# Optimization experiments

Hardware: AMD Instinct MI355X
Metric: run time of the kernel (lower is better)

Reference implementation:

```python
import jax, jax.numpy as jnp
import numpy as np

N_NODES = 50000
IN_CH = 512
OUT_CH = 512
N_EDGES = 800000


def setup_inputs() -> dict:
    key = jax.random.key(0)
    ks = jax.random.split(key, 6)
    x = jax.random.normal(ks[0], (N_NODES, IN_CH), dtype=jnp.float32)
    edge_index = jax.random.randint(ks[1], (2, N_EDGES), 0, N_NODES, dtype=jnp.int64)
    edge_index_2 = jax.random.randint(ks[2], (2, N_EDGES), 0, N_NODES, dtype=jnp.int64)
    W1 = jax.random.normal(ks[3], (IN_CH, OUT_CH), dtype=jnp.float32) * (1.0 / np.sqrt(IN_CH))
    b1 = jnp.zeros((OUT_CH,), dtype=jnp.float32)
    W2 = jax.random.normal(ks[4], (IN_CH, OUT_CH), dtype=jnp.float32) * (1.0 / np.sqrt(IN_CH))
    b2 = jnp.zeros((OUT_CH,), dtype=jnp.float32)
    return {"x": x, "edge_index": edge_index, "edge_index_2": edge_index_2,
            "W1": W1, "b1": b1, "W2": W2, "b2": b2}


def _sgconv(x, edge_index, W, b, K=2):
    # PyG SGConv: K rounds of D^-1/2 (A+I) D^-1/2 propagation, then Linear.
    N = x.shape[0]
    loops = jnp.arange(N, dtype=edge_index.dtype)
    row = jnp.concatenate([edge_index[0], loops])  # source nodes
    col = jnp.concatenate([edge_index[1], loops])  # destination nodes
    deg = jax.ops.segment_sum(jnp.ones_like(col, dtype=x.dtype), col, num_segments=N)
    deg_inv_sqrt = jnp.where(deg > 0, jnp.where(deg > 0, deg, 1.0) ** -0.5, 0.0)
    norm = deg_inv_sqrt[row] * deg_inv_sqrt[col]  # [E+N]
    h = x
    for _ in range(K):
        h = jax.ops.segment_sum(h[row] * norm[:, None], col, num_segments=N)
    return h @ W + b


def reference(x, edge_index, edge_index_2, W1, b1, W2, b2):
    x1 = _sgconv(x, edge_index, W1, b1)
    x2 = _sgconv(x, edge_index_2, W2, b2)
    logits = jax.nn.softmax(x1, axis=1)
    logits_2 = jax.nn.softmax(x2, axis=1)
    predictions = jnp.argmax(logits, axis=1)
    return (logits, logits_2, predictions)
```

## Files before the change

kernel.cpp:

```cpp
#include <hip/hip_runtime.h>
#include <hip/hip_bf16.h>
#include <cstdint>
#include <cstddef>

#define N_NODES 50000
#define N_EDGES 800000
#define CH 512
#define SCAN_NB 49

typedef __attribute__((ext_vector_type(8))) short bf16x8;
typedef __attribute__((ext_vector_type(4))) float f32x4;

__device__ inline unsigned short f2b(float f) {
    __hip_bfloat16 h = __float2bfloat16(f);
    return *(unsigned short*)&h;
}
__device__ inline float blo(unsigned int u) {
    union { unsigned int i; float f; } v; v.i = u << 16; return v.f;
}
__device__ inline float bhi(unsigned int u) {
    union { unsigned int i; float f; } v; v.i = u & 0xffff0000u; return v.f;
}
__device__ inline unsigned int pack2(unsigned short a, unsigned short b) {
    return (unsigned)a | ((unsigned)b << 16);
}


__global__ __launch_bounds__(256) void count_both(const int* __restrict__ e1, const int* __restrict__ e2,
                                                  int* __restrict__ cnt1, int* __restrict__ cnt2) {
    int t = blockIdx.x * 256 + threadIdx.x;
    if (t < N_EDGES) {
        atomicAdd(&cnt1[e1[N_EDGES + t]], 1);
    } else if (t < 2 * N_EDGES) {
        int e = t - N_EDGES;
        atomicAdd(&cnt2[e2[N_EDGES + e]], 1);
    }
}

__global__ __launch_bounds__(256) void scan_s1(const int* __restrict__ c1, const int* __restrict__ c2,
                                               int* __restrict__ o1, int* __restrict__ o2,
                                               int* __restrict__ bsum) {
    const int* cnt = blockIdx.y ? c2 : c1;
    int* offs = blockIdx.y ? o2 : o1;
    int* bs = bsum + blockIdx.y * 64;
    int b = blockIdx.x, tid = threadIdx.x;
    int lane = tid & 63, wid = tid >> 6;
    int i0 = b * 1024 + tid * 4;
    int v[4];
    #pragma unroll
    for (int j = 0; j < 4; ++j) { int i = i0 + j; v[j] = (i < N_NODES) ? cnt[i] : 0; }
    int tsum = v[0] + v[1] + v[2] + v[3];
    int incl = tsum;
    #pragma unroll
    for (int d = 1; d < 64; d <<= 1) {
        int t = __shfl_up(incl, d, 64);
        if (lane >= d) incl += t;
    }
    __shared__ int wsum[4];
    if (lane == 63) wsum[wid] = incl;
    __syncthreads();
    int wbase = 0;
    for (int w = 0; w < wid; ++w) wbase += wsum[w];
    int run = wbase + incl - tsum;
    #pragma unroll
    for (int j = 0; j < 4; ++j) { int i = i0 + j; if (i < N_NODES) offs[i] = run; run += v[j]; }
    if (tid == 255) bs[b] = wbase + incl;
}

__global__ __launch_bounds__(64) void scan_s2(int* __restrict__ bsum,
                                              int* __restrict__ o1, int* __restrict__ o2) {
    int* bs = bsum + blockIdx.y * 64;
    int* offs = blockIdx.y ? o2 : o1;
    int t = threadIdx.x;
    int v = (t < SCAN_NB) ? bs[t] : 0;
    int incl = v;
    #pragma unroll
    for (int d = 1; d < 64; d <<= 1) {
        int u = __shfl_up(incl, d, 64);
        if (t >= d) incl += u;
    }
    if (t < SCAN_NB) bs[t] = incl - v;
    if (t == 63) offs[N_NODES] = incl;
}

__global__ __launch_bounds__(256) void scan_s3(const int* __restrict__ c1, const int* __restrict__ c2,
                                               int* __restrict__ o1, int* __restrict__ o2,
                                               float* __restrict__ d1, float* __restrict__ d2,
                                               int* __restrict__ cur1, int* __restrict__ cur2,
                                               const int* __restrict__ bsum) {
    const int* cnt = blockIdx.y ? c2 : c1;
    int* offs = blockIdx.y ? o2 : o1;
    float* dinv = blockIdx.y ? d2 : d1;
    int* cursor = blockIdx.y ? cur2 : cur1;
    int add = bsum[blockIdx.y * 64 + blockIdx.x];
    int i0 = blockIdx.x * 1024 + threadIdx.x * 4;
    #pragma unroll
    for (int j = 0; j < 4; ++j) {
        int i = i0 + j;
        if (i < N_NODES) {
            offs[i] += add;
            dinv[i] = rsqrtf((float)(cnt[i] + 1));
            cursor[i] = 0;
        }
    }
}

__global__ __launch_bounds__(256) void fill_both(const int* __restrict__ e1,
                                                 const int* __restrict__ offs1, int* __restrict__ cur1,
                                                 const float* __restrict__ dinv1,
                                                 int* __restrict__ srcs1, float* __restrict__ enorm1,
                                                 const int* __restrict__ e2,
                                                 const int* __restrict__ offs2, int* __restrict__ cur2,
                                                 const float* __restrict__ dinv2,
                                                 int* __restrict__ srcs2, float* __restrict__ enorm2) {
    int t = blockIdx.x * 256 + threadIdx.x;
    if (t < N_EDGES) {
        int r = e1[t];
        int c = e1[N_EDGES + t];
        int p = offs1[c] + atomicAdd(&cur1[c], 1);
        srcs1[p] = r;
        enorm1[p] = dinv1[r] * dinv1[c];
    } else if (t < 2 * N_EDGES) {
        int e = t - N_EDGES;
        int r = e2[e];
        int c = e2[N_EDGES + e];
        int p = offs2[c] + atomicAdd(&cur2[c], 1);
        srcs2[p] = r;
        enorm2[p] = dinv2[r] * dinv2[c];
    }
}


__global__ __launch_bounds__(256) void convert_x_bf16(const float* __restrict__ x, unsigned short* __restrict__ xb) {
    int i8 = blockIdx.x * 256 + threadIdx.x;
    const float4* x4 = (const float4*)x;
    float4 a = x4[2 * i8], b = x4[2 * i8 + 1];
    unsigned int o[4];
    o[0] = pack2(f2b(a.x), f2b(a.y));
    o[1] = pack2(f2b(a.z), f2b(a.w));
    o[2] = pack2(f2b(b.x), f2b(b.y));
    o[3] = pack2(f2b(b.z), f2b(b.w));
    ((uint4*)xb)[i8] = make_uint4(o[0], o[1], o[2], o[3]);
}

__global__ __launch_bounds__(256) void convert_w_t(const float* __restrict__ W, unsigned short* __restrict__ Wt) {
    int id = blockIdx.x * 256 + threadIdx.x;
    int k = id >> 9, n = id & 511;
    Wt[(size_t)n * 512 + k] = f2b(W[(size_t)k * 512 + n]);
}

__global__ __launch_bounds__(256) void convert_w_t_split(const float* __restrict__ W,
                                                         unsigned short* __restrict__ Wth,
                                                         unsigned short* __restrict__ Wtl) {
    int id = blockIdx.x * 256 + threadIdx.x;
    int k = id >> 9, n = id & 511;
    float f = W[(size_t)k * 512 + n];
    unsigned short hb = f2b(f);
    union { unsigned int u; float ff; } t; t.u = (unsigned)hb << 16;
    float lo = f - t.ff;
    Wth[(size_t)n * 512 + k] = hb;
    Wtl[(size_t)n * 512 + k] = f2b(lo);
}


__global__ __launch_bounds__(128) void propagate(const float* __restrict__ h, float* __restrict__ out,
                                                 const int* __restrict__ offs,
                                                 const int* __restrict__ srcs,
                                                 const float* __restrict__ enorm,
                                                 const float* __restrict__ dinv) {
    int node = blockIdx.x;
    int t = threadIdx.x;
    const float4* h4 = (const float4*)h;
    float di = dinv[node];
    float w0 = di * di;
    float4 v = h4[(size_t)node * 128 + t];
    float4 acc = make_float4(v.x * w0, v.y * w0, v.z * w0, v.w * w0);
    int e0 = offs[node], e1 = offs[node + 1];
    int e = e0;
    int eu = e0 + ((e1 - e0) & ~7);
    for (; e < eu; e += 8) {
        int s[8]; float w[8];
        #pragma unroll
        for (int q = 0; q < 8; ++q) { s[q] = srcs[e + q]; w[q] = enorm[e + q]; }
        float4 u[8];
        #pragma unroll
        for (int q = 0; q < 8; ++q) u[q] = h4[(size_t)s[q] * 128 + t];
        #pragma unroll
        for (int q = 0; q < 8; ++q) {
            acc.x += u[q].x * w[q]; acc.y += u[q].y * w[q];
            acc.z += u[q].z * w[q]; acc.w += u[q].w * w[q];
        }
    }
    for (; e < e1; ++e) {
        int s = srcs[e];
        float w = enorm[e];
        float4 u = h4[(size_t)s * 128 + t];
        acc.x += u.x * w; acc.y += u.y * w; acc.z += u.z * w; acc.w += u.w * w;
    }
    ((float4*)out)[(size_t)node * 128 + t] = acc;
}


__global__ __launch_bounds__(128) void propagate_bf16(const unsigned short* __restrict__ hb,
                                                      unsigned short* __restrict__ outb,
                                                      const int* __restrict__ offs,
                                                      const int* __restrict__ srcs,
                                                      const float* __restrict__ enorm,
                                                      const float* __restrict__ dinv) {
    int node = blockIdx.x * 2 + (threadIdx.x >> 6);
    int lane = threadIdx.x & 63;
    const uint4* h16 = (const uint4*)hb;
    float di = dinv[node];
    float w0 = di * di;
    float acc[8];
    uint4 sv = h16[(size_t)node * 64 + lane];
    acc[0] = blo(sv.x) * w0; acc[1] = bhi(sv.x) * w0;
    acc[2] = blo(sv.y) * w0; acc[3] = bhi(sv.y) * w0;
    acc[4] = blo(sv.z) * w0; acc[5] = bhi(sv.z) * w0;
    acc[6] = blo(sv.w) * w0; acc[7] = bhi(sv.w) * w0;
    int e0 = offs[node], e1 = offs[node + 1];
    int e = e0;
    int eu = e0 + ((e1 - e0) & ~7);
    for (; e < eu; e += 8) {
        int s[8]; float w[8];
        #pragma unroll
        for (int q = 0; q < 8; ++q) { s[q] = srcs[e + q]; w[q] = enorm[e + q]; }
        uint4 u[8];
        #pragma unroll
        for (int q = 0; q < 8; ++q) u[q] = h16[(size_t)s[q] * 64 + lane];
        #pragma unroll
        for (int q = 0; q < 8; ++q) {
            acc[0] += blo(u[q].x) * w[q]; acc[1] += bhi(u[q].x) * w[q];
            acc[2] += blo(u[q].y) * w[q]; acc[3] += bhi(u[q].y) * w[q];
            acc[4] += blo(u[q].z) * w[q]; acc[5] += bhi(u[q].z) * w[q];
            acc[6] += blo(u[q].w) * w[q]; acc[7] += bhi(u[q].w) * w[q];
        }
    }
    for (; e < e1; ++e) {
        int s = srcs[e];
        float w = enorm[e];
        uint4 u = h16[(size_t)s * 64 + lane];
        acc[0] += blo(u.x) * w; acc[1] += bhi(u.x) * w;
        acc[2] += blo(u.y) * w; acc[3] += bhi(u.y) * w;
        acc[4] += blo(u.z) * w; acc[5] += bhi(u.z) * w;
        acc[6] += blo(u.w) * w; acc[7] += bhi(u.w) * w;
    }
    unsigned int o0 = pack2(f2b(acc[0]), f2b(acc[1]));
    unsigned int o1 = pack2(f2b(acc[2]), f2b(acc[3]));
    unsigned int o2 = pack2(f2b(acc[4]), f2b(acc[5]));
    unsigned int o3 = pack2(f2b(acc[6]), f2b(acc[7]));
    ((uint4*)outb)[(size_t)node * 64 + lane] = make_uint4(o0, o1, o2, o3);
}


#define BM2 128
#define BN2 256
#define BK2 32
#define LDP 40

__global__ __launch_bounds__(512) void gemm_bf16(const unsigned short* __restrict__ Ab,
                                                 const unsigned short* __restrict__ Wt,
                                                 const float* __restrict__ bias,
                                                 float* __restrict__ C) {
    __shared__ short Alds[BM2 * LDP];
    __shared__ short Blds[BN2 * LDP];
    int tid = threadIdx.x;
    int lane = tid & 63;
    int wid = tid >> 6;
    int wm = wid & 1;
    int wn = wid >> 1;
    int bm = blockIdx.x * BM2;
    int bn = blockIdx.y * BN2;

    f32x4 acc[4][4] = {};

    int arow = tid >> 2, ak8 = (tid & 3) * 8;
    int brow = tid >> 1, bk16 = (tid & 1) * 16;
    int ga = bm + arow;
    bool aval = ga < N_NODES;

    for (int k0 = 0; k0 < CH; k0 += BK2) {
        {
            uint4 v = make_uint4(0u, 0u, 0u, 0u);
            if (aval) v = *(const uint4*)&Ab[(size_t)ga * CH + k0 + ak8];
            *(uint4*)&Alds[arow * LDP + ak8] = v;
        }
        {
            const unsigned short* s = &Wt[(size_t)(bn + brow) * CH + k0 + bk16];
            *(uint4*)&Blds[brow * LDP + bk16] = *(const uint4*)s;
            *(uint4*)&Blds[brow * LDP + bk16 + 8] = *(const uint4*)(s + 8);
        }
        __syncthreads();

        bf16x8 af[4], bf[4];
        #pragma unroll
        for (int mt = 0; mt < 4; ++mt)
            af[mt] = *(const bf16x8*)&Alds[(wm * 64 + mt * 16 + (lane & 15)) * LDP + (lane >> 4) * 8];
        #pragma unroll
        for (int nt = 0; nt < 4; ++nt)
            bf[nt] = *(const bf16x8*)&Blds[(wn * 64 + nt * 16 + (lane & 15)) * LDP + (lane >> 4) * 8];
        #pragma unroll
        for (int mt = 0; mt < 4; ++mt)
            #pragma unroll
            for (int nt = 0; nt < 4; ++nt)
                acc[mt][nt] = __builtin_amdgcn_mfma_f32_16x16x32_bf16(af[mt], bf[nt], acc[mt][nt], 0, 0, 0);
        __syncthreads();
    }

    #pragma unroll
    for (int mt = 0; mt < 4; ++mt) {
        #pragma unroll
        for (int nt = 0; nt < 4; ++nt) {
            int col = bn + wn * 64 + nt * 16 + (lane & 15);
            float bv = bias[col];
            #pragma unroll
            for (int r = 0; r < 4; ++r) {
                int row = bm + wm * 64 + mt * 16 + (lane >> 4) * 4 + r;
                if (row < N_NODES) C[(size_t)row * CH + col] = acc[mt][nt][r] + bv;
            }
        }
    }
}


#define BM3 128
#define BN3 256
#define BK3 32
#define LDP3 40

__global__ __launch_bounds__(512) void gemm_bf16x3(const float* __restrict__ A,
                                                   const unsigned short* __restrict__ Wth,
                                                   const unsigned short* __restrict__ Wtl,
                                                   const float* __restrict__ bias,
                                                   float* __restrict__ C) {
    __shared__ short Ah[BM3 * LDP3];
    __shared__ short Al[BM3 * LDP3];
    __shared__ short Bh[BN3 * LDP3];
    __shared__ short Bl[BN3 * LDP3];
    int tid = threadIdx.x;
    int lane = tid & 63;
    int wid = tid >> 6;
    int wm = wid & 1;
    int wn = wid >> 1;
    int bm = blockIdx.x * BM3;
    int bn = blockIdx.y * BN3;

    f32x4 acc[4][4] = {};

    int arow = tid >> 2, ak8 = (tid & 3) * 8;
    int brow = tid >> 1, bk16 = (tid & 1) * 16;
    int ga = bm + arow;
    bool aval = ga < N_NODES;

    for (int k0 = 0; k0 < CH; k0 += BK3) {
        {
            const float* src = &A[(size_t)ga * CH + k0 + ak8];
            float4 f0 = aval ? *(const float4*)(src)     : make_float4(0.f, 0.f, 0.f, 0.f);
            float4 f1 = aval ? *(const float4*)(src + 4) : make_float4(0.f, 0.f, 0.f, 0.f);
            float fs[8] = {f0.x, f0.y, f0.z, f0.w, f1.x, f1.y, f1.z, f1.w};
            unsigned short h[8], l[8];
            #pragma unroll
            for (int j = 0; j < 8; ++j) {
                unsigned short hb = f2b(fs[j]);
                union { unsigned int u; float ff; } t; t.u = (unsigned)hb << 16;
                float lo = fs[j] - t.ff;
                h[j] = hb;
                l[j] = f2b(lo);
            }
            *(uint4*)&Ah[arow * LDP3 + ak8] =
                make_uint4(pack2(h[0], h[1]), pack2(h[2], h[3]), pack2(h[4], h[5]), pack2(h[6], h[7]));
            *(uint4*)&Al[arow * LDP3 + ak8] =
                make_uint4(pack2(l[0], l[1]), pack2(l[2], l[3]), pack2(l[4], l[5]), pack2(l[6], l[7]));
        }
        {
            const unsigned short* sh = &Wth[(size_t)(bn + brow) * CH + k0 + bk16];
            const unsigned short* sl = &Wtl[(size_t)(bn + brow) * CH + k0 + bk16];
            *(uint4*)&Bh[brow * LDP3 + bk16]     = *(const uint4*)sh;
            *(uint4*)&Bh[brow * LDP3 + bk16 + 8] = *(const uint4*)(sh + 8);
            *(uint4*)&Bl[brow * LDP3 + bk16]     = *(const uint4*)sl;
            *(uint4*)&Bl[brow * LDP3 + bk16 + 8] = *(const uint4*)(sl + 8);
        }
        __syncthreads();

        bf16x8 afh[4], afl[4], bfh[4], bfl[4];
        #pragma unroll
        for (int mt = 0; mt < 4; ++mt) {
            int off = (wm * 64 + mt * 16 + (lane & 15)) * LDP3 + (lane >> 4) * 8;
            afh[mt] = *(const bf16x8*)&Ah[off];
            afl[mt] = *(const bf16x8*)&Al[off];
        }
        #pragma unroll
        for (int nt = 0; nt < 4; ++nt) {
            int off = (wn * 64 + nt * 16 + (lane & 15)) * LDP3 + (lane >> 4) * 8;
            bfh[nt] = *(const bf16x8*)&Bh[off];
            bfl[nt] = *(const bf16x8*)&Bl[off];
        }
        #pragma unroll
        for (int mt = 0; mt < 4; ++mt)
            #pragma unroll
            for (int nt = 0; nt < 4; ++nt) {
                acc[mt][nt] = __builtin_amdgcn_mfma_f32_16x16x32_bf16(afh[mt], bfh[nt], acc[mt][nt], 0, 0, 0);
                acc[mt][nt] = __builtin_amdgcn_mfma_f32_16x16x32_bf16(afl[mt], bfh[nt], acc[mt][nt], 0, 0, 0);
                acc[mt][nt] = __builtin_amdgcn_mfma_f32_16x16x32_bf16(afh[mt], bfl[nt], acc[mt][nt], 0, 0, 0);
            }
        __syncthreads();
    }

    #pragma unroll
    for (int mt = 0; mt < 4; ++mt) {
        #pragma unroll
        for (int nt = 0; nt < 4; ++nt) {
            int col = bn + wn * 64 + nt * 16 + (lane & 15);
            float bv = bias[col];
            #pragma unroll
            for (int r = 0; r < 4; ++r) {
                int row = bm + wm * 64 + mt * 16 + (lane >> 4) * 4 + r;
                if (row < N_NODES) C[(size_t)row * CH + col] = acc[mt][nt][r] + bv;
            }
        }
    }
}


#define GAP_THR 2.0e-4f
#define SUSP_CAP 49999

__global__ __launch_bounds__(256) void softmax_rows(const float* __restrict__ X, float* __restrict__ P,
                                                    float* __restrict__ preds,
                                                    int* __restrict__ susp_cnt,
                                                    int* __restrict__ susp_rows) {
    int row = blockIdx.x * 4 + (threadIdx.x >> 6);
    int lane = threadIdx.x & 63;
    if (row >= N_NODES) return;
    const float4* x4 = (const float4*)(X + (size_t)row * CH);
    float4 v0 = x4[lane];
    float4 v1 = x4[lane + 64];
    float vals[8] = {v0.x, v0.y, v0.z, v0.w, v1.x, v1.y, v1.z, v1.w};
    float m = vals[0];
    float m2 = -INFINITY;
    int mi = lane * 4;
    #pragma unroll
    for (int j = 1; j < 8; ++j) {
        int c = (j < 4) ? (lane * 4 + j) : (256 + lane * 4 + (j - 4));
        if (vals[j] > m) { m2 = m; m = vals[j]; mi = c; }
        else if (vals[j] > m2) { m2 = vals[j]; }
    }
    #pragma unroll
    for (int d = 32; d > 0; d >>= 1) {
        float om = __shfl_xor(m, d, 64);
        int oi = __shfl_xor(mi, d, 64);
        float om2 = __shfl_xor(m2, d, 64);
        if (om > m || (om == m && oi < mi)) {
            m2 = fmaxf(m, om2);
            m = om; mi = oi;
        } else {
            m2 = fmaxf(m2, om);
        }
    }
    float s = 0.f;
    float ex[8];
    #pragma unroll
    for (int j = 0; j < 8; ++j) { ex[j] = __expf(vals[j] - m); s += ex[j]; }
    #pragma unroll
    for (int d = 32; d > 0; d >>= 1) s += __shfl_xor(s, d, 64);
    float inv = 1.0f / s;
    float4 o0 = make_float4(ex[0] * inv, ex[1] * inv, ex[2] * inv, ex[3] * inv);
    float4 o1 = make_float4(ex[4] * inv, ex[5] * inv, ex[6] * inv, ex[7] * inv);
    float4* p4 = (float4*)(P + (size_t)row * CH);
    p4[lane] = o0;
    p4[lane + 64] = o1;
    if (preds != nullptr && lane == 0) {
        preds[row] = (float)mi;
        if (m - m2 < GAP_THR) {
            int p = atomicAdd(susp_cnt, 1);
            if (p < SUSP_CAP) susp_rows[p] = row;
        }
    }
}


__global__ __launch_bounds__(256) void fix_preds(const float* __restrict__ A, const float* __restrict__ W,
                                                 const float* __restrict__ bias,
                                                 const int* __restrict__ susp_cnt,
                                                 const int* __restrict__ susp_rows,
                                                 float* __restrict__ preds) {
    __shared__ float rowbuf[8][512];
    __shared__ float rbest[8][4];
    __shared__ int ridx[8][4];
    int cnt = *susp_cnt;
    if (cnt > SUSP_CAP) cnt = SUSP_CAP;
    int tid = threadIdx.x, lane = tid & 63, wid = tid >> 6;
    for (int base = blockIdx.x * 8; base < cnt; base += gridDim.x * 8) {
        int nr = min(8, cnt - base);
        __syncthreads();
        for (int r = 0; r < nr; ++r) {
            int row = susp_rows[base + r];
            if (tid < 128) ((float4*)rowbuf[r])[tid] = ((const float4*)&A[(size_t)row * 512])[tid];
        }
        __syncthreads();
        float best[8]; int bidx[8];
        #pragma unroll
        for (int r = 0; r < 8; ++r) { best[r] = -INFINITY; bidx[r] = 0; }
        for (int cc = 0; cc < 2; ++cc) {
            int c = cc * 256 + tid;
            float bv = bias[c];
            float s[8];
            #pragma unroll
            for (int r = 0; r < 8; ++r) s[r] = bv;
            #pragma unroll 8
            for (int k = 0; k < 512; ++k) {
                float w = W[(size_t)k * 512 + c];
                #pragma unroll
                for (int r = 0; r < 8; ++r) s[r] += rowbuf[r][k] * w;
            }
            #pragma unroll
            for (int r = 0; r < 8; ++r)
                if (s[r] > best[r]) { best[r] = s[r]; bidx[r] = c; }
        }
        #pragma unroll
        for (int r = 0; r < 8; ++r) {
            float b = best[r]; int i = bidx[r];
            #pragma unroll
            for (int d = 32; d > 0; d >>= 1) {
                float ob = __shfl_xor(b, d, 64);
                int oi = __shfl_xor(i, d, 64);
                if (ob > b || (ob == b && oi < i)) { b = ob; i = oi; }
            }
            if (lane == 0) { rbest[r][wid] = b; ridx[r][wid] = i; }
        }
        __syncthreads();
        if (tid < nr) {
            int r = tid;
            float b = rbest[r][0]; int i = ridx[r][0];
            #pragma unroll
            for (int w = 1; w < 4; ++w) {
                if (rbest[r][w] > b || (rbest[r][w] == b && ridx[r][w] < i)) { b = rbest[r][w]; i = ridx[r][w]; }
            }
            preds[susp_rows[base + r]] = (float)i;
        }
    }
}


extern "C" void kernel_launch(void* const* d_in, const int* in_sizes, int n_in,
                              void* d_out, int out_size, void* d_ws, size_t ws_size,
                              hipStream_t stream) {
    const float* x  = (const float*)d_in[0];
    const int*   e1 = (const int*)d_in[1];
    const int*   e2 = (const int*)d_in[2];
    const float* W1 = (const float*)d_in[3];
    const float* b1 = (const float*)d_in[4];
    const float* W2 = (const float*)d_in[5];
    const float* b2 = (const float*)d_in[6];

    float* out     = (float*)d_out;
    float* logits1 = out;
    float* logits2 = out + (size_t)N_NODES * CH;
    float* preds   = out + 2 * (size_t)N_NODES * CH;

    const size_t NEED = 109600016;
    if (ws_size < NEED) return;

    char* ws = (char*)d_ws;
    float* A       = (float*)(ws);
    int*   cnt1    = (int*)(ws + 102400000);
    int*   offs1   = (int*)(ws + 102600000);
    int*   cursor1 = (int*)(ws + 102800016);
    float* dinv1   = (float*)(ws + 103000016);
    int*   srcs1   = (int*)(ws + 103200016);
    float* enorm1  = (float*)(ws + 106400016);

    char* L2 = (char*)logits2;
    int*   cnt2    = (int*)(L2);
    int*   offs2   = (int*)(L2 + 200000);
    int*   cursor2 = (int*)(L2 + 400016);
    float* dinv2   = (float*)(L2 + 600016);
    int*   srcs2   = (int*)(L2 + 800016);
    float* enorm2  = (float*)(L2 + 4000016);
    int*   bsum    = (int*)(L2 + 7200016);

    unsigned short* xb  = (unsigned short*)logits1;
    unsigned short* Wtb = (unsigned short*)((char*)logits1 + 51200000);
    unsigned short* h1b = (unsigned short*)A;
    unsigned short* h2b = (unsigned short*)((char*)A + 51200000);

    unsigned short* Wt1h = (unsigned short*)srcs1;
    unsigned short* Wt1l = (unsigned short*)enorm1;
    int* susp_cnt  = (int*)cursor1;
    int* susp_rows = (int*)cursor1 + 1;

    {
        hipMemsetAsync(cnt1, 0, N_NODES * sizeof(int), stream);
        hipMemsetAsync(cnt2, 0, N_NODES * sizeof(int), stream);
        count_both<<<(2 * N_EDGES + 255) / 256, 256, 0, stream>>>(e1, e2, cnt1, cnt2);
        scan_s1<<<dim3(SCAN_NB, 2), 256, 0, stream>>>(cnt1, cnt2, offs1, offs2, bsum);
        scan_s2<<<dim3(1, 2), 64, 0, stream>>>(bsum, offs1, offs2);
        scan_s3<<<dim3(SCAN_NB, 2), 256, 0, stream>>>(cnt1, cnt2, offs1, offs2,
                                                      dinv1, dinv2, cursor1, cursor2, bsum);
        fill_both<<<(2 * N_EDGES + 255) / 256, 256, 0, stream>>>(
            e1, offs1, cursor1, dinv1, srcs1, enorm1,
            e2, offs2, cursor2, dinv2, srcs2, enorm2);
    }

    {
        convert_x_bf16<<<(N_NODES * CH / 8 + 255) / 256, 256, 0, stream>>>(x, xb);
        convert_w_t<<<(512 * 512) / 256, 256, 0, stream>>>(W2, Wtb);

        propagate_bf16<<<N_NODES / 2, 128, 0, stream>>>(xb, h1b, offs2, srcs2, enorm2, dinv2);
        propagate_bf16<<<N_NODES / 2, 128, 0, stream>>>(h1b, h2b, offs2, srcs2, enorm2, dinv2);

        dim3 g((N_NODES + BM2 - 1) / BM2, CH / BN2);
        gemm_bf16<<<g, 512, 0, stream>>>(h2b, Wtb, b2, logits2);
        softmax_rows<<<N_NODES / 4, 256, 0, stream>>>(logits2, logits2, nullptr, nullptr, nullptr);
    }

    {
        propagate<<<N_NODES, 128, 0, stream>>>(x, logits1, offs1, srcs1, enorm1, dinv1);
        propagate<<<N_NODES, 128, 0, stream>>>(logits1, A, offs1, srcs1, enorm1, dinv1);

        convert_w_t_split<<<(512 * 512) / 256, 256, 0, stream>>>(W1, Wt1h, Wt1l);
        hipMemsetAsync(susp_cnt, 0, sizeof(int), stream);

        dim3 g((N_NODES + BM3 - 1) / BM3, CH / BN3);
        gemm_bf16x3<<<g, 512, 0, stream>>>(A, Wt1h, Wt1l, b1, logits1);
        softmax_rows<<<N_NODES / 4, 256, 0, stream>>>(logits1, logits1, preds, susp_cnt, susp_rows);
        fix_preds<<<400, 256, 0, stream>>>(A, W1, b1, susp_cnt, susp_rows, preds);
    }
}
```

Measured before the change: 1.561 ms.

## Fuse branch-2 GEMM and softmax with branch-1 propagation via block-range kernels

Merges the bf16 GEMM for the second SGConv with the first fp32 propagation round into one launch, where block ranges select which work each block does. It also merges the second-branch softmax with the second fp32 propagation round. The goal is to let the compute-bound GEMM overlap with the memory-bound gather, and to fill the GPU during the small softmax. Buffers are re-aliased (Wtb moves into A), and the propagate kernel now runs 4 nodes per 512-thread block, which changes its occupancy profile.

```diff
diff --git a/kernel.cpp b/kernel.cpp
--- a/kernel.cpp
+++ b/kernel.cpp
@@ -163,13 +163,10 @@
 }
 
 
-__global__ __launch_bounds__(128) void propagate(const float* __restrict__ h, float* __restrict__ out,
-                                                 const int* __restrict__ offs,
-                                                 const int* __restrict__ srcs,
-                                                 const float* __restrict__ enorm,
-                                                 const float* __restrict__ dinv) {
-    int node = blockIdx.x;
-    int t = threadIdx.x;
+__device__ inline void prop_node(const float* __restrict__ h, float* __restrict__ out,
+                                 const int* __restrict__ offs, const int* __restrict__ srcs,
+                                 const float* __restrict__ enorm, const float* __restrict__ dinv,
+                                 int node, int t) {
     const float4* h4 = (const float4*)h;
     float di = dinv[node];
     float w0 = di * di;
@@ -257,20 +254,30 @@
 #define BN2 256
 #define BK2 32
 #define LDP 40
-
-__global__ __launch_bounds__(512) void gemm_bf16(const unsigned short* __restrict__ Ab,
-                                                 const unsigned short* __restrict__ Wt,
-                                                 const float* __restrict__ bias,
-                                                 float* __restrict__ C) {
+#define GEMM2_GX 391
+#define GEMM2_BLOCKS (GEMM2_GX * 2)
+#define PROP_BLOCKS 12500
+
+__global__ __launch_bounds__(512) void fused_gemm2_prop1(
+        const unsigned short* __restrict__ Ab, const unsigned short* __restrict__ Wt,
+        const float* __restrict__ bias, float* __restrict__ C,
+        const float* __restrict__ hx, float* __restrict__ pout,
+        const int* __restrict__ offs, const int* __restrict__ srcs,
+        const float* __restrict__ enorm, const float* __restrict__ dinv) {
     __shared__ short Alds[BM2 * LDP];
     __shared__ short Blds[BN2 * LDP];
     int tid = threadIdx.x;
+    if (blockIdx.x >= GEMM2_BLOCKS) {
+        int node = (blockIdx.x - GEMM2_BLOCKS) * 4 + (tid >> 7);
+        prop_node(hx, pout, offs, srcs, enorm, dinv, node, tid & 127);
+        return;
+    }
     int lane = tid & 63;
     int wid = tid >> 6;
     int wm = wid & 1;
     int wn = wid >> 1;
-    int bm = blockIdx.x * BM2;
-    int bn = blockIdx.y * BN2;
+    int bm = (blockIdx.x % GEMM2_GX) * BM2;
+    int bn = (blockIdx.x / GEMM2_GX) * BN2;
 
     f32x4 acc[4][4] = {};
 
@@ -320,6 +327,45 @@
             }
         }
     }
+}
+
+
+#define SM2_BLOCKS 6250
+
+__global__ __launch_bounds__(512) void fused_sm2_prop2(
+        float* __restrict__ X,
+        const float* __restrict__ hin, float* __restrict__ aout,
+        const int* __restrict__ offs, const int* __restrict__ srcs,
+        const float* __restrict__ enorm, const float* __restrict__ dinv) {
+    int tid = threadIdx.x;
+    if (blockIdx.x >= SM2_BLOCKS) {
+        int node = (blockIdx.x - SM2_BLOCKS) * 4 + (tid >> 7);
+        prop_node(hin, aout, offs, srcs, enorm, dinv, node, tid & 127);
+        return;
+    }
+    int row = blockIdx.x * 8 + (tid >> 6);
+    int lane = tid & 63;
+    const float4* x4 = (const float4*)(X + (size_t)row * CH);
+    float4 v0 = x4[lane];
+    float4 v1 = x4[lane + 64];
+    float vals[8] = {v0.x, v0.y, v0.z, v0.w, v1.x, v1.y, v1.z, v1.w};
+    float m = vals[0];
+    #pragma unroll
+    for (int j = 1; j < 8; ++j) m = fmaxf(m, vals[j]);
+    #pragma unroll
+    for (int d = 32; d > 0; d >>= 1) m = fmaxf(m, __shfl_xor(m, d, 64));
+    float s = 0.f;
+    float ex[8];
+    #pragma unroll
+    for (int j = 0; j < 8; ++j) { ex[j] = __expf(vals[j] - m); s += ex[j]; }
+    #pragma unroll
+    for (int d = 32; d > 0; d >>= 1) s += __shfl_xor(s, d, 64);
+    float inv = 1.0f / s;
+    float4 o0 = make_float4(ex[0] * inv, ex[1] * inv, ex[2] * inv, ex[3] * inv);
+    float4 o1 = make_float4(ex[4] * inv, ex[5] * inv, ex[6] * inv, ex[7] * inv);
+    float4* p4 = (float4*)(X + (size_t)row * CH);
+    p4[lane] = o0;
+    p4[lane + 64] = o1;
 }
 
 
@@ -580,50 +626,45 @@
     int*   bsum    = (int*)(L2 + 7200016);
 
     unsigned short* xb  = (unsigned short*)logits1;
-    unsigned short* Wtb = (unsigned short*)((char*)logits1 + 51200000);
     unsigned short* h1b = (unsigned short*)A;
     unsigned short* h2b = (unsigned short*)((char*)A + 51200000);
+    unsigned short* Wtb = (unsigned short*)A;
 
     unsigned short* Wt1h = (unsigned short*)srcs1;
     unsigned short* Wt1l = (unsigned short*)enorm1;
     int* susp_cnt  = (int*)cursor1;
     int* susp_rows = (int*)cursor1 + 1;
 
-    {
-        hipMemsetAsync(cnt1, 0, N_NODES * sizeof(int), stream);
-        hipMemsetAsync(cnt2, 0, N_NODES * sizeof(int), stream);
-        count_both<<<(2 * N_EDGES + 255) / 256, 256, 0, stream>>>(e1, e2, cnt1, cnt2);
-        scan_s1<<<dim3(SCAN_NB, 2), 256, 0, stream>>>(cnt1, cnt2, offs1, offs2, bsum);
-        scan_s2<<<dim3(1, 2), 64, 0, stream>>>(bsum, offs1, offs2);
-        scan_s3<<<dim3(SCAN_NB, 2), 256, 0, stream>>>(cnt1, cnt2, offs1, offs2,
-                                                      dinv1, dinv2, cursor1, cursor2, bsum);
-        fill_both<<<(2 * N_EDGES + 255) / 256, 256, 0, stream>>>(
-            e1, offs1, cursor1, dinv1, srcs1, enorm1,
-            e2, offs2, cursor2, dinv2, srcs2, enorm2);
-    }
-
-    {
-        convert_x_bf16<<<(N_NODES * CH / 8 + 255) / 256, 256, 0, stream>>>(x, xb);
-        convert_w_t<<<(512 * 512) / 256, 256, 0, stream>>>(W2, Wtb);
-
-        propagate_bf16<<<N_NODES / 2, 128, 0, stream>>>(xb, h1b, offs2, srcs2, enorm2, dinv2);
-        propagate_bf16<<<N_NODES / 2, 128, 0, stream>>>(h1b, h2b, offs2, srcs2, enorm2, dinv2);
-
-        dim3 g((N_NODES + BM2 - 1) / BM2, CH / BN2);
-        gemm_bf16<<<g, 512, 0, stream>>>(h2b, Wtb, b2, logits2);
-        softmax_rows<<<N_NODES / 4, 256, 0, stream>>>(logits2, logits2, nullptr, nullptr, nullptr);
-    }
-
-    {
-        propagate<<<N_NODES, 128, 0, stream>>>(x, logits1, offs1, srcs1, enorm1, dinv1);
-        propagate<<<N_NODES, 128, 0, stream>>>(logits1, A, offs1, srcs1, enorm1, dinv1);
-
-        convert_w_t_split<<<(512 * 512) / 256, 256, 0, stream>>>(W1, Wt1h, Wt1l);
-        hipMemsetAsync(susp_cnt, 0, sizeof(int), stream);
-
-        dim3 g((N_NODES + BM3 - 1) / BM3, CH / BN3);
-        gemm_bf16x3<<<g, 512, 0, stream>>>(A, Wt1h, Wt1l, b1, logits1);
-        softmax_rows<<<N_NODES / 4, 256, 0, stream>>>(logits1, logits1, preds, susp_cnt, susp_rows);
-        fix_preds<<<400, 256, 0, stream>>>(A, W1, b1, susp_cnt, susp_rows, preds);
-    }
-}
+    hipMemsetAsync(cnt1, 0, N_NODES * sizeof(int), stream);
+    hipMemsetAsync(cnt2, 0, N_NODES * sizeof(int), stream);
+    count_both<<<(2 * N_EDGES + 255) / 256, 256, 0, stream>>>(e1, e2, cnt1, cnt2);
+    scan_s1<<<dim3(SCAN_NB, 2), 256, 0, stream>>>(cnt1, cnt2, offs1, offs2, bsum);
+    scan_s2<<<dim3(1, 2), 64, 0, stream>>>(bsum, offs1, offs2);
+    scan_s3<<<dim3(SCAN_NB, 2), 256, 0, stream>>>(cnt1, cnt2, offs1, offs2,
+                                                  dinv1, dinv2, cursor1, cursor2, bsum);
+    fill_both<<<(2 * N_EDGES + 255) / 256, 256, 0, stream>>>(
+        e1, offs1, cursor1, dinv1, srcs1, enorm1,
+        e2, offs2, cursor2, dinv2, srcs2, enorm2);
+
+    convert_x_bf16<<<(N_NODES * CH / 8 + 255) / 256, 256, 0, stream>>>(x, xb);
+    propagate_bf16<<<N_NODES / 2, 128, 0, stream>>>(xb, h1b, offs2, srcs2, enorm2, dinv2);
+    propagate_bf16<<<N_NODES / 2, 128, 0, stream>>>(h1b, h2b, offs2, srcs2, enorm2, dinv2);
+
+    convert_w_t<<<(512 * 512) / 256, 256, 0, stream>>>(W2, Wtb);
+
+    fused_gemm2_prop1<<<GEMM2_BLOCKS + PROP_BLOCKS, 512, 0, stream>>>(
+        h2b, Wtb, b2, logits2,
+        x, logits1, offs1, srcs1, enorm1, dinv1);
+
+    fused_sm2_prop2<<<SM2_BLOCKS + PROP_BLOCKS, 512, 0, stream>>>(
+        logits2,
+        logits1, A, offs1, srcs1, enorm1, dinv1);
+
+    convert_w_t_split<<<(512 * 512) / 256, 256, 0, stream>>>(W1, Wt1h, Wt1l);
+    hipMemsetAsync(susp_cnt, 0, sizeof(int), stream);
+
+    dim3 g((N_NODES + BM3 - 1) / BM3, CH / BN3);
+    gemm_bf16x3<<<g, 512, 0, stream>>>(A, Wt1h, Wt1l, b1, logits1);
+    softmax_rows<<<N_NODES / 4, 256, 0, stream>>>(logits1, logits1, preds, susp_cnt, susp_rows);
+    fix_preds<<<400, 256, 0, stream>>>(A, W1, b1, susp_cnt, susp_rows, preds);
+}
```

After: 1.512 ms. 3.2% less time.
